# Kernel tuning notes

Measured on AMD Instinct MI355X. Metric: run time of the kernel, lower is better.

Reference implementation:

```python
import jax, jax.numpy as jnp
import numpy as np

WINDOW = 128  # window_size from init_kwargs
D = 1024      # input_dim
S = 8192      # seq_len


def setup_inputs() -> dict:
    key = jax.random.key(0)
    k1, k2, k3, k4, k5 = jax.random.split(key, 5)
    bound = 1.0 / np.sqrt(D)
    x = jax.random.normal(k1, (1, S, D), dtype=jnp.float32)
    Wq = jax.random.uniform(k2, (D, D), minval=-bound, maxval=bound, dtype=jnp.float32)
    bq = jax.random.uniform(k3, (D,), minval=-bound, maxval=bound, dtype=jnp.float32)
    Wk = jax.random.uniform(k4, (D, D), minval=-bound, maxval=bound, dtype=jnp.float32)
    bk = jax.random.uniform(k5, (D,), minval=-bound, maxval=bound, dtype=jnp.float32)
    return {"x": x, "Wq": Wq, "bq": bq, "Wk": Wk, "bk": bk}


def reference(x, Wq, bq, Wk, bk):
    # x: [1, S, D]  (original code only works with batch==1)
    xs = x[0]                          # [S, D]
    q = xs @ Wq.T + bq                 # [S, D]
    k = xs @ Wk.T + bk                 # [S, D]
    scores = q @ k.T                   # [S, S] dense, matches original buffer
    t = jnp.arange(S)[:, None]
    s = jnp.arange(S)[None, :]
    # original writes scores only for s in [t-WINDOW, t+WINDOW); elsewhere stays 0
    inwin = (s >= t - WINDOW) & (s < t + WINDOW)
    scores = jnp.where(inwin, scores, 0.0)
    attn = jax.nn.softmax(scores, axis=1)  # softmax INCLUDES the zero entries, as in original
    out = attn @ xs                    # [S, D]
    return out
```

## Files before the change

### kernel.cpp

```cpp
#include <hip/hip_runtime.h>

#define S 8192
#define D 1024
#define WINDOW 128
#define TQ 16
#define UMAX 288
#define BK 32
#define PAD 68
#define BAND 384

typedef __attribute__((ext_vector_type(8))) short short8;
typedef __attribute__((ext_vector_type(4))) float floatx4;
typedef __attribute__((ext_vector_type(4))) unsigned short ushort4v;
typedef unsigned short u16t;

__device__ __forceinline__ float wave_sum(float v) {
  #pragma unroll
  for (int off = 32; off > 0; off >>= 1) v += __shfl_xor(v, off, 64);
  return v;
}
__device__ __forceinline__ float wave_max(float v) {
  #pragma unroll
  for (int off = 32; off > 0; off >>= 1) v = fmaxf(v, __shfl_xor(v, off, 64));
  return v;
}
__device__ __forceinline__ unsigned int f2bf_rn(float f) {
  unsigned int u = __float_as_uint(f);
  return (u + 0x7fffu + ((u >> 16) & 1u)) >> 16;
}

__global__ __launch_bounds__(256) void uv_kernel(
    const float* __restrict__ Wq, const float* __restrict__ Wk,
    const float* __restrict__ bq, const float* __restrict__ bk,
    float* __restrict__ u, float* __restrict__ v, float* __restrict__ cbuf)
{
  const int i = blockIdx.x * 256 + threadIdx.x;
  const int n0 = blockIdx.y * 128;
  float us = 0.f, vs = 0.f;
  for (int n = n0; n < n0 + 128; ++n) {
    us += Wq[(size_t)n * D + i] * bk[n];
    vs += Wk[(size_t)n * D + i] * bq[n];
  }
  atomicAdd(&u[i], us);
  atomicAdd(&v[i], vs);
  if (blockIdx.x == 0 && blockIdx.y == 0) {
    float cs = 0.f;
    for (int n = threadIdx.x; n < D; n += 256) cs += bq[n] * bk[n];
    atomicAdd(cbuf, cs);
  }
}

__global__ __launch_bounds__(256) void prep_kernel(
    const float* __restrict__ x, const float* __restrict__ u,
    const float* __restrict__ v, u16t* __restrict__ xhi, u16t* __restrict__ xlo,
    u16t* __restrict__ xT, float* __restrict__ xsum,
    float* __restrict__ a, float* __restrict__ b)
{
  __shared__ float tile[64][65];
  const int s0 = blockIdx.x * 64;
  const int d0 = blockIdx.y * 64;
  const int t = threadIdx.x;
  #pragma unroll
  for (int p = 0; p < 4; ++p) {
    int r = (t >> 4) + p * 16;
    int c = (t & 15) * 4;
    float4 vv = *(const float4*)(x + (size_t)(s0 + r) * D + d0 + c);
    float f[4] = {vv.x, vv.y, vv.z, vv.w};
    tile[r][c+0] = vv.x; tile[r][c+1] = vv.y; tile[r][c+2] = vv.z; tile[r][c+3] = vv.w;
    ushort4v h, l;
    #pragma unroll
    for (int e = 0; e < 4; ++e) {
      unsigned int hb = f2bf_rn(f[e]);
      float hf = __uint_as_float(hb << 16);
      h[e] = (u16t)hb;
      l[e] = (u16t)f2bf_rn(f[e] - hf);
    }
    size_t idx = (size_t)(s0 + r) * D + d0 + c;
    *(ushort4v*)(xhi + idx) = h;
    *(ushort4v*)(xlo + idx) = l;
  }
  __syncthreads();
  #pragma unroll
  for (int p = 0; p < 4; ++p) {
    int dd = (t >> 4) + p * 16;
    int ss = (t & 15) * 4;
    ushort4v o;
    #pragma unroll
    for (int e = 0; e < 4; ++e) o[e] = (u16t)f2bf_rn(tile[ss + e][dd]);
    *(ushort4v*)(xT + (size_t)(d0 + dd) * S + s0 + ss) = o;
  }
  if (t < 64) {
    float s = 0.f;
    #pragma unroll 8
    for (int r = 0; r < 64; ++r) s += tile[r][t];
    atomicAdd(&xsum[d0 + t], s);
  } else if (t < 128) {
    int r = t - 64;
    float s = 0.f;
    for (int c = 0; c < 64; ++c) s += tile[r][c] * u[d0 + c];
    atomicAdd(&a[s0 + r], s);
  } else if (t < 192) {
    int r = t - 128;
    float s = 0.f;
    for (int c = 0; c < 64; ++c) s += tile[r][c] * v[d0 + c];
    atomicAdd(&b[s0 + r], s);
  }
}

__global__ __launch_bounds__(256) void transposeW_kernel(
    const float* __restrict__ Wq, const float* __restrict__ Wk,
    u16t* __restrict__ wqth, u16t* __restrict__ wqtl,
    u16t* __restrict__ wkth, u16t* __restrict__ wktl)
{
  __shared__ float tile[64][65];
  const float* W = blockIdx.z ? Wk : Wq;
  u16t* oh = blockIdx.z ? wkth : wqth;
  u16t* ol = blockIdx.z ? wktl : wqtl;
  const int n0 = blockIdx.x * 64;
  const int i0 = blockIdx.y * 64;
  const int t = threadIdx.x;
  #pragma unroll
  for (int p = 0; p < 4; ++p) {
    int r = (t >> 4) + p * 16;
    int c = (t & 15) * 4;
    float4 vv = *(const float4*)(W + (size_t)(n0 + r) * D + i0 + c);
    tile[r][c+0] = vv.x; tile[r][c+1] = vv.y; tile[r][c+2] = vv.z; tile[r][c+3] = vv.w;
  }
  __syncthreads();
  #pragma unroll
  for (int p = 0; p < 4; ++p) {
    int ii = (t >> 4) + p * 16;
    int nn = (t & 15) * 4;
    ushort4v h, l;
    #pragma unroll
    for (int e = 0; e < 4; ++e) {
      float f = tile[nn + e][ii];
      unsigned int hb = f2bf_rn(f);
      float hf = __uint_as_float(hb << 16);
      h[e] = (u16t)hb;
      l[e] = (u16t)f2bf_rn(f - hf);
    }
    size_t idx = (size_t)(i0 + ii) * D + n0 + nn;
    *(ushort4v*)(oh + idx) = h;
    *(ushort4v*)(ol + idx) = l;
  }
}

__global__ __launch_bounds__(256) void m_kernel(
    const u16t* __restrict__ wqth, const u16t* __restrict__ wqtl,
    const u16t* __restrict__ wkth, const u16t* __restrict__ wktl,
    u16t* __restrict__ mh, u16t* __restrict__ ml)
{
  __shared__ __align__(16) u16t Mbuf[4][64 * BK];

  const int tid  = threadIdx.x;
  const int lane = tid & 63;
  const int wv   = tid >> 6;
  const int i0   = blockIdx.x * 64;
  const int j0   = blockIdx.y * 64;

  floatx4 acc[2][2] = {};
  const int m0w = (wv & 1) * 32;
  const int n0w = (wv >> 1) * 32;
  const int srow = lane >> 2;
  const int scol = (lane & 3) * 8;

  for (int k0 = 0; k0 < D; k0 += BK) {
    __syncthreads();
    {
      const u16t* src = (wv == 0) ? wqth : (wv == 1) ? wqtl : (wv == 2) ? wkth : wktl;
      const int base  = (wv < 2) ? i0 : j0;
      #pragma unroll
      for (int sg = 0; sg < 4; ++sg) {
        int row = base + sg * 16 + srow;
        size_t g = (size_t)row * D + k0 + scol;
        __builtin_amdgcn_global_load_lds(
            (const __attribute__((address_space(1))) void*)(src + g),
            (__attribute__((address_space(3))) void*)(&Mbuf[wv][sg * 512]), 16, 0, 0);
      }
    }
    __syncthreads();
    short8 ah[2], al[2], bh[2], bl[2];
    #pragma unroll
    for (int t = 0; t < 2; ++t) {
      int ar = (m0w + t * 16 + (lane & 15)) * BK + (lane >> 4) * 8;
      int br = (n0w + t * 16 + (lane & 15)) * BK + (lane >> 4) * 8;
      ah[t] = *(const short8*)&Mbuf[0][ar];
      al[t] = *(const short8*)&Mbuf[1][ar];
      bh[t] = *(const short8*)&Mbuf[2][br];
      bl[t] = *(const short8*)&Mbuf[3][br];
    }
    #pragma unroll
    for (int mt = 0; mt < 2; ++mt)
      #pragma unroll
      for (int nt = 0; nt < 2; ++nt) {
        acc[mt][nt] = __builtin_amdgcn_mfma_f32_16x16x32_bf16(ah[mt], bh[nt], acc[mt][nt], 0, 0, 0);
        acc[mt][nt] = __builtin_amdgcn_mfma_f32_16x16x32_bf16(ah[mt], bl[nt], acc[mt][nt], 0, 0, 0);
        acc[mt][nt] = __builtin_amdgcn_mfma_f32_16x16x32_bf16(al[mt], bh[nt], acc[mt][nt], 0, 0, 0);
      }
  }
  #pragma unroll
  for (int mt = 0; mt < 2; ++mt)
    #pragma unroll
    for (int nt = 0; nt < 2; ++nt) {
      int j = j0 + n0w + nt * 16 + (lane & 15);
      int i = i0 + m0w + mt * 16 + (lane >> 4) * 4;
      #pragma unroll
      for (int r = 0; r < 4; ++r) {
        float f = acc[mt][nt][r];
        unsigned int hb = f2bf_rn(f);
        float hf = __uint_as_float(hb << 16);
        size_t idx = (size_t)(i + r) * D + j;
        mh[idx] = (u16t)hb;
        ml[idx] = (u16t)f2bf_rn(f - hf);
      }
    }
}

__global__ __launch_bounds__(256) void y_kernel(
    const u16t* __restrict__ xhi, const u16t* __restrict__ xlo,
    const u16t* __restrict__ mhp, const u16t* __restrict__ mlp,
    u16t* __restrict__ yh, u16t* __restrict__ yl)
{
  __shared__ __align__(16) u16t Ah[2 * 128 * BK];
  __shared__ __align__(16) u16t Al[2 * 128 * BK];
  __shared__ __align__(16) u16t Bh[2 * 128 * BK];
  __shared__ __align__(16) u16t Bl[2 * 128 * BK];

  const int tid  = threadIdx.x;
  const int lane = tid & 63;
  const int wv   = tid >> 6;
  const int s0   = blockIdx.x * 128;
  const int i0   = blockIdx.y * 128;

  floatx4 acc[4][4] = {};
  const int m0w  = (wv & 1) * 64;
  const int n0w  = (wv >> 1) * 64;
  const int srow = lane >> 2;
  const int scol = (lane & 3) * 8;

  for (int k0 = 0; k0 < D; k0 += 64) {
    __syncthreads();
    #pragma unroll
    for (int h = 0; h < 2; ++h) {
      #pragma unroll
      for (int sg = 0; sg < 2; ++sg) {
        int seg  = wv * 2 + sg;
        int arow = s0 + seg * 16 + srow;
        int brow = i0 + seg * 16 + srow;
        size_t ga = (size_t)arow * D + k0 + h * 32 + scol;
        size_t gb = (size_t)brow * D + k0 + h * 32 + scol;
        int lb = h * 4096 + seg * 512;
        __builtin_amdgcn_global_load_lds(
            (const __attribute__((address_space(1))) void*)(xhi + ga),
            (__attribute__((address_space(3))) void*)(&Ah[lb]), 16, 0, 0);
        __builtin_amdgcn_global_load_lds(
            (const __attribute__((address_space(1))) void*)(xlo + ga),
            (__attribute__((address_space(3))) void*)(&Al[lb]), 16, 0, 0);
        __builtin_amdgcn_global_load_lds(
            (const __attribute__((address_space(1))) void*)(mhp + gb),
            (__attribute__((address_space(3))) void*)(&Bh[lb]), 16, 0, 0);
        __builtin_amdgcn_global_load_lds(
            (const __attribute__((address_space(1))) void*)(mlp + gb),
            (__attribute__((address_space(3))) void*)(&Bl[lb]), 16, 0, 0);
      }
    }
    __syncthreads();
    #pragma unroll
    for (int h = 0; h < 2; ++h) {
      short8 ah[4], al[4], bh[4], bl[4];
      #pragma unroll
      for (int t = 0; t < 4; ++t) {
        int ar = h * 4096 + (m0w + t * 16 + (lane & 15)) * BK + (lane >> 4) * 8;
        int br = h * 4096 + (n0w + t * 16 + (lane & 15)) * BK + (lane >> 4) * 8;
        ah[t] = *(const short8*)&Ah[ar];
        al[t] = *(const short8*)&Al[ar];
        bh[t] = *(const short8*)&Bh[br];
        bl[t] = *(const short8*)&Bl[br];
      }
      #pragma unroll
      for (int mt = 0; mt < 4; ++mt)
        #pragma unroll
        for (int nt = 0; nt < 4; ++nt) {
          acc[mt][nt] = __builtin_amdgcn_mfma_f32_16x16x32_bf16(ah[mt], bh[nt], acc[mt][nt], 0, 0, 0);
          acc[mt][nt] = __builtin_amdgcn_mfma_f32_16x16x32_bf16(ah[mt], bl[nt], acc[mt][nt], 0, 0, 0);
          acc[mt][nt] = __builtin_amdgcn_mfma_f32_16x16x32_bf16(al[mt], bh[nt], acc[mt][nt], 0, 0, 0);
        }
    }
  }
  #pragma unroll
  for (int mt = 0; mt < 4; ++mt)
    #pragma unroll
    for (int nt = 0; nt < 4; ++nt) {
      int i = i0 + n0w + nt * 16 + (lane & 15);
      int s = s0 + m0w + mt * 16 + (lane >> 4) * 4;
      #pragma unroll
      for (int r = 0; r < 4; ++r) {
        float f = acc[mt][nt][r];
        unsigned int hb = f2bf_rn(f);
        float hf = __uint_as_float(hb << 16);
        size_t idx = (size_t)(s + r) * D + i;
        yh[idx] = (u16t)hb;
        yl[idx] = (u16t)f2bf_rn(f - hf);
      }
    }
}

__global__ __launch_bounds__(256) void scores_kernel(
    const u16t* __restrict__ xhi, const u16t* __restrict__ xlo,
    const u16t* __restrict__ yh, const u16t* __restrict__ yl,
    const float* __restrict__ a, const float* __restrict__ b,
    const float* __restrict__ cbuf, float* __restrict__ band)
{
  __shared__ __align__(16) u16t Ah[2 * 128 * BK];
  __shared__ __align__(16) u16t Al[2 * 128 * BK];
  __shared__ __align__(16) u16t Bh[2 * 128 * BK];
  __shared__ __align__(16) u16t Bl[2 * 128 * BK];

  const int tid  = threadIdx.x;
  const int lane = tid & 63;
  const int wv   = tid >> 6;
  const int t0   = blockIdx.x * 128;
  const int jt   = blockIdx.y;
  const int s_base = t0 - 128 + jt * 128;
  const float cval = cbuf[0];

  floatx4 acc[4][4] = {};
  const int m0w  = (wv & 1) * 64;
  const int n0w  = (wv >> 1) * 64;
  const int srow = lane >> 2;
  const int scol = (lane & 3) * 8;

  for (int k0 = 0; k0 < D; k0 += 64) {
    __syncthreads();
    #pragma unroll
    for (int h = 0; h < 2; ++h) {
      #pragma unroll
      for (int sg = 0; sg < 2; ++sg) {
        int seg  = wv * 2 + sg;
        int arow = t0 + seg * 16 + srow;
        int brow = s_base + seg * 16 + srow;
        brow = min(max(brow, 0), S - 1);
        size_t ga = (size_t)arow * D + k0 + h * 32 + scol;
        size_t gb = (size_t)brow * D + k0 + h * 32 + scol;
        int lb = h * 4096 + seg * 512;
        __builtin_amdgcn_global_load_lds(
            (const __attribute__((address_space(1))) void*)(xhi + ga),
            (__attribute__((address_space(3))) void*)(&Ah[lb]), 16, 0, 0);
        __builtin_amdgcn_global_load_lds(
            (const __attribute__((address_space(1))) void*)(xlo + ga),
            (__attribute__((address_space(3))) void*)(&Al[lb]), 16, 0, 0);
        __builtin_amdgcn_global_load_lds(
            (const __attribute__((address_space(1))) void*)(yh + gb),
            (__attribute__((address_space(3))) void*)(&Bh[lb]), 16, 0, 0);
        __builtin_amdgcn_global_load_lds(
            (const __attribute__((address_space(1))) void*)(yl + gb),
            (__attribute__((address_space(3))) void*)(&Bl[lb]), 16, 0, 0);
      }
    }
    __syncthreads();
    #pragma unroll
    for (int h = 0; h < 2; ++h) {
      short8 ah[4], al[4], bh[4], bl[4];
      #pragma unroll
      for (int t = 0; t < 4; ++t) {
        int ar = h * 4096 + (m0w + t * 16 + (lane & 15)) * BK + (lane >> 4) * 8;
        int br = h * 4096 + (n0w + t * 16 + (lane & 15)) * BK + (lane >> 4) * 8;
        ah[t] = *(const short8*)&Ah[ar];
        al[t] = *(const short8*)&Al[ar];
        bh[t] = *(const short8*)&Bh[br];
        bl[t] = *(const short8*)&Bl[br];
      }
      #pragma unroll
      for (int mt = 0; mt < 4; ++mt)
        #pragma unroll
        for (int nt = 0; nt < 4; ++nt) {
          acc[mt][nt] = __builtin_amdgcn_mfma_f32_16x16x32_bf16(ah[mt], bh[nt], acc[mt][nt], 0, 0, 0);
          acc[mt][nt] = __builtin_amdgcn_mfma_f32_16x16x32_bf16(ah[mt], bl[nt], acc[mt][nt], 0, 0, 0);
          acc[mt][nt] = __builtin_amdgcn_mfma_f32_16x16x32_bf16(al[mt], bh[nt], acc[mt][nt], 0, 0, 0);
        }
    }
  }
  #pragma unroll
  for (int mt = 0; mt < 4; ++mt)
    #pragma unroll
    for (int nt = 0; nt < 4; ++nt) {
      int n_loc = n0w + nt * 16 + (lane & 15);
      int s = s_base + n_loc;
      float bv = (s >= 0 && s < S) ? b[s] : 0.f;
      #pragma unroll
      for (int r = 0; r < 4; ++r) {
        int m_loc = m0w + mt * 16 + (lane >> 4) * 4 + r;
        int t = t0 + m_loc;
        bool inwin = (s >= t - WINDOW) && (s < t + WINDOW) && (s >= 0) && (s < S);
        float sv = inwin ? (acc[mt][nt][r] + a[t] + bv + cval) : 0.f;
        band[(size_t)t * BAND + jt * 128 + n_loc] = sv;
      }
    }
}

__global__ __launch_bounds__(256) void softmax_kernel(
    const float* __restrict__ band, u16t* __restrict__ Pb, float* __restrict__ e0d)
{
  const int lane = threadIdx.x & 63;
  const int w    = threadIdx.x >> 6;
  const int t    = blockIdx.x * 4 + w;
  const float* row = band + (size_t)t * BAND;
  float v[6];
  float mx = 0.f;
  #pragma unroll
  for (int i = 0; i < 6; ++i) {
    v[i] = row[i * 64 + lane];
    mx = fmaxf(mx, v[i]);
  }
  mx = wave_max(mx);
  float e0 = __expf(-mx);
  float ss = 0.f;
  #pragma unroll
  for (int i = 0; i < 6; ++i) {
    v[i] = __expf(v[i] - mx);
    ss += v[i];
  }
  ss = wave_sum(ss);
  float dinv = 1.f / (ss + (float)(S - BAND) * e0);
  #pragma unroll
  for (int i = 0; i < 6; ++i)
    Pb[(size_t)t * BAND + i * 64 + lane] = (u16t)f2bf_rn((v[i] - e0) * dinv);
  if (lane == 0) e0d[t] = e0 * dinv;
}

__global__ __launch_bounds__(256) void pv_kernel(
    const u16t* __restrict__ Pb, const u16t* __restrict__ xT,
    const float* __restrict__ e0d, const float* __restrict__ xsum,
    float* __restrict__ out)
{
  __shared__ __align__(16) u16t Ab[2 * 128 * BK];
  __shared__ __align__(16) u16t Bb[2 * 128 * BK];

  const int tid  = threadIdx.x;
  const int lane = tid & 63;
  const int wv   = tid >> 6;
  const int t0   = blockIdx.x * 128;
  const int d0   = blockIdx.y * 128;
  const int origin = t0 - 128;

  floatx4 acc[4][4] = {};
  const int m0w  = (wv & 1) * 64;
  const int n0w  = (wv >> 1) * 64;
  const int srow = lane >> 2;
  const int scol = (lane & 3) * 8;

  for (int k0 = 0; k0 < BAND; k0 += 64) {
    __syncthreads();
    #pragma unroll
    for (int h = 0; h < 2; ++h) {
      #pragma unroll
      for (int sg = 0; sg < 2; ++sg) {
        int seg  = wv * 2 + sg;
        int arow = t0 + seg * 16 + srow;
        int brow = d0 + seg * 16 + srow;
        int s_g  = origin + k0 + h * 32 + scol;
        s_g = min(max(s_g, 0), S - 8);
        size_t ga = (size_t)arow * BAND + k0 + h * 32 + scol;
        size_t gb = (size_t)brow * S + s_g;
        int lb = h * 4096 + seg * 512;
        __builtin_amdgcn_global_load_lds(
            (const __attribute__((address_space(1))) void*)(Pb + ga),
            (__attribute__((address_space(3))) void*)(&Ab[lb]), 16, 0, 0);
        __builtin_amdgcn_global_load_lds(
            (const __attribute__((address_space(1))) void*)(xT + gb),
            (__attribute__((address_space(3))) void*)(&Bb[lb]), 16, 0, 0);
      }
    }
    __syncthreads();
    #pragma unroll
    for (int h = 0; h < 2; ++h) {
      short8 af[4], bf[4];
      #pragma unroll
      for (int t = 0; t < 4; ++t) {
        int ar = h * 4096 + (m0w + t * 16 + (lane & 15)) * BK + (lane >> 4) * 8;
        int br = h * 4096 + (n0w + t * 16 + (lane & 15)) * BK + (lane >> 4) * 8;
        af[t] = *(const short8*)&Ab[ar];
        bf[t] = *(const short8*)&Bb[br];
      }
      #pragma unroll
      for (int mt = 0; mt < 4; ++mt)
        #pragma unroll
        for (int nt = 0; nt < 4; ++nt)
          acc[mt][nt] = __builtin_amdgcn_mfma_f32_16x16x32_bf16(af[mt], bf[nt], acc[mt][nt], 0, 0, 0);
    }
  }
  #pragma unroll
  for (int mt = 0; mt < 4; ++mt)
    #pragma unroll
    for (int nt = 0; nt < 4; ++nt) {
      int n_g = d0 + n0w + nt * 16 + (lane & 15);
      float xs = xsum[n_g];
      #pragma unroll
      for (int r = 0; r < 4; ++r) {
        int m_g = t0 + m0w + mt * 16 + (lane >> 4) * 4 + r;
        out[(size_t)m_g * D + n_g] = acc[mt][nt][r] + e0d[m_g] * xs;
      }
    }
}

__global__ __launch_bounds__(256) void proj_kernel(
    const float* __restrict__ x, const float* __restrict__ Wq,
    const float* __restrict__ bqv, const float* __restrict__ Wk,
    const float* __restrict__ bkv, float* __restrict__ qout,
    float* __restrict__ kout)
{
  __shared__ __align__(16) float xs[BK][PAD];
  __shared__ __align__(16) float wqs[BK][PAD];
  __shared__ __align__(16) float wks[BK][PAD];
  const int tid = threadIdx.x;
  const int tx = tid & 15, ty = tid >> 4;
  const int t0 = blockIdx.x * 64, i0 = blockIdx.y * 64;
  float accq[4][4] = {}, acck[4][4] = {};
  const int lrow0 = tid >> 3, lc4 = (tid & 7) * 4;
  for (int k0 = 0; k0 < D; k0 += BK) {
    __syncthreads();
    #pragma unroll
    for (int p = 0; p < 2; ++p) {
      int row = lrow0 + p * 32;
      float4 a = *(const float4*)(x  + (size_t)(t0 + row) * D + k0 + lc4);
      float4 b = *(const float4*)(Wq + (size_t)(i0 + row) * D + k0 + lc4);
      float4 c = *(const float4*)(Wk + (size_t)(i0 + row) * D + k0 + lc4);
      xs [lc4+0][row]=a.x; xs [lc4+1][row]=a.y; xs [lc4+2][row]=a.z; xs [lc4+3][row]=a.w;
      wqs[lc4+0][row]=b.x; wqs[lc4+1][row]=b.y; wqs[lc4+2][row]=b.z; wqs[lc4+3][row]=b.w;
      wks[lc4+0][row]=c.x; wks[lc4+1][row]=c.y; wks[lc4+2][row]=c.z; wks[lc4+3][row]=c.w;
    }
    __syncthreads();
    #pragma unroll
    for (int kk = 0; kk < BK; ++kk) {
      float4 av = *(const float4*)&xs [kk][ty*4];
      float4 bv = *(const float4*)&wqs[kk][tx*4];
      float4 cv = *(const float4*)&wks[kk][tx*4];
      float a[4] = {av.x, av.y, av.z, av.w};
      float b[4] = {bv.x, bv.y, bv.z, bv.w};
      float c[4] = {cv.x, cv.y, cv.z, cv.w};
      #pragma unroll
      for (int r = 0; r < 4; ++r)
        #pragma unroll
        for (int cc = 0; cc < 4; ++cc) {
          accq[r][cc] = fmaf(a[r], b[cc], accq[r][cc]);
          acck[r][cc] = fmaf(a[r], c[cc], acck[r][cc]);
        }
    }
  }
  float4 bq4 = *(const float4*)(bqv + i0 + tx*4);
  float4 bk4 = *(const float4*)(bkv + i0 + tx*4);
  #pragma unroll
  for (int r = 0; r < 4; ++r) {
    int trow = t0 + ty*4 + r;
    float4 oq = { accq[r][0]+bq4.x, accq[r][1]+bq4.y, accq[r][2]+bq4.z, accq[r][3]+bq4.w };
    float4 ok = { acck[r][0]+bk4.x, acck[r][1]+bk4.y, acck[r][2]+bk4.z, acck[r][3]+bk4.w };
    *(float4*)(qout + (size_t)trow * D + i0 + tx*4) = oq;
    *(float4*)(kout + (size_t)trow * D + i0 + tx*4) = ok;
  }
}

__global__ __launch_bounds__(256) void colsum_kernel(const float* __restrict__ x,
                                                     float* __restrict__ xsum)
{
  int d = blockIdx.x * 256 + threadIdx.x;
  int tbase = blockIdx.y * 256;
  float s = 0.f;
  for (int t = 0; t < 256; ++t) s += x[(size_t)(tbase + t) * D + d];
  atomicAdd(&xsum[d], s);
}

__global__ __launch_bounds__(256) void attn_kernel(
    const float* __restrict__ x, const float* __restrict__ q,
    const float* __restrict__ kmat, const float* __restrict__ xsum,
    float* __restrict__ out)
{
  __shared__ __align__(16) float scl[TQ][UMAX];
  __shared__ float e0s[TQ], dinv[TQ];
  const int tid = threadIdx.x, lane = tid & 63, wv = tid >> 6;
  const int t0 = blockIdx.x * TQ;
  const int lo_u = max(0, t0 - WINDOW);
  const int hi_u = min(S, t0 + TQ - 1 + WINDOW);
  const int ucnt = hi_u - lo_u;
  for (int i = tid; i < TQ * UMAX; i += 256) (&scl[0][0])[i] = 0.f;
  __syncthreads();
  {
    const int tiB = wv * 4;
    float4 qf[4][4];
    #pragma unroll
    for (int g = 0; g < 4; ++g) {
      int t = t0 + tiB + g;
      #pragma unroll
      for (int j = 0; j < 4; ++j)
        qf[g][j] = *(const float4*)(q + (size_t)t * D + lane*4 + j*256);
    }
    const int wlo = max(0, t0 + tiB - WINDOW);
    const int whi = min(S, t0 + tiB + 3 + WINDOW);
    for (int s = wlo; s < whi; ++s) {
      float4 kf[4];
      #pragma unroll
      for (int j = 0; j < 4; ++j)
        kf[j] = *(const float4*)(kmat + (size_t)s * D + lane*4 + j*256);
      float acc[4];
      #pragma unroll
      for (int g = 0; g < 4; ++g) {
        float v = 0.f;
        #pragma unroll
        for (int j = 0; j < 4; ++j) {
          v = fmaf(qf[g][j].x, kf[j].x, v);
          v = fmaf(qf[g][j].y, kf[j].y, v);
          v = fmaf(qf[g][j].z, kf[j].z, v);
          v = fmaf(qf[g][j].w, kf[j].w, v);
        }
        acc[g] = v;
      }
      #pragma unroll
      for (int g = 0; g < 4; ++g) {
        float tot = wave_sum(acc[g]);
        int t = t0 + tiB + g;
        if (lane == 0 && s >= t - WINDOW && s < t + WINDOW)
          scl[tiB + g][s - lo_u] = tot;
      }
    }
  }
  __syncthreads();
  #pragma unroll
  for (int g = 0; g < 4; ++g) {
    int ti = wv * 4 + g;
    int t = t0 + ti;
    int lo = max(0, t - WINDOW), hi = min(S, t + WINDOW);
    int cnt = hi - lo, off = lo - lo_u;
    float m = 0.f;
    for (int i = lane; i < cnt; i += 64) m = fmaxf(m, scl[ti][off + i]);
    m = wave_max(m);
    float e0 = __expf(-m);
    float ssum = 0.f;
    for (int i = lane; i < cnt; i += 64) {
      float e = __expf(scl[ti][off + i] - m);
      ssum += e;
      scl[ti][off + i] = e - e0;
    }
    ssum = wave_sum(ssum);
    if (lane == 0) {
      dinv[ti] = 1.f / (ssum + (float)(S - cnt) * e0);
      e0s[ti] = e0;
    }
  }
  __syncthreads();
  {
    const int c4 = tid * 4;
    float4 acc[TQ];
    #pragma unroll
    for (int ti = 0; ti < TQ; ++ti) acc[ti] = make_float4(0.f, 0.f, 0.f, 0.f);
    for (int su = 0; su < ucnt; su += 4) {
      float4 xr[4];
      #pragma unroll
      for (int u = 0; u < 4; ++u)
        xr[u] = *(const float4*)(x + (size_t)(lo_u + su + u) * D + c4);
      #pragma unroll
      for (int ti = 0; ti < TQ; ++ti) {
        float4 w4 = *(const float4*)&scl[ti][su];
        float wvv[4] = {w4.x, w4.y, w4.z, w4.w};
        #pragma unroll
        for (int u = 0; u < 4; ++u) {
          acc[ti].x = fmaf(wvv[u], xr[u].x, acc[ti].x);
          acc[ti].y = fmaf(wvv[u], xr[u].y, acc[ti].y);
          acc[ti].z = fmaf(wvv[u], xr[u].z, acc[ti].z);
          acc[ti].w = fmaf(wvv[u], xr[u].w, acc[ti].w);
        }
      }
    }
    float4 xsv = *(const float4*)(xsum + c4);
    #pragma unroll
    for (int ti = 0; ti < TQ; ++ti) {
      float e0 = e0s[ti], di = dinv[ti];
      float4 o;
      o.x = (acc[ti].x + e0 * xsv.x) * di;
      o.y = (acc[ti].y + e0 * xsv.y) * di;
      o.z = (acc[ti].z + e0 * xsv.z) * di;
      o.w = (acc[ti].w + e0 * xsv.w) * di;
      *(float4*)(out + (size_t)(t0 + ti) * D + c4) = o;
    }
  }
}

extern "C" void kernel_launch(void* const* d_in, const int* in_sizes, int n_in,
                              void* d_out, int out_size, void* d_ws, size_t ws_size,
                              hipStream_t stream) {
  const float* x  = (const float*)d_in[0];
  const float* Wq = (const float*)d_in[1];
  const float* bq = (const float*)d_in[2];
  const float* Wk = (const float*)d_in[3];
  const float* bk = (const float*)d_in[4];
  float* outp = (float*)d_out;

  const size_t SD = (size_t)S * D;
  const size_t DD = (size_t)D * D;

  float* xsum = (float*)d_ws;
  float* u    = xsum + D;
  float* v    = u + D;
  float* a    = v + D;
  float* b    = a + S;
  float* cbuf = b + S;
  size_t zero_bytes = (size_t)(3 * D + 2 * S + 16) * sizeof(float);

  u16t* xhi  = (u16t*)(cbuf + 16);
  u16t* xlo  = xhi + SD;
  u16t* xT   = xlo + SD;
  u16t* wqth = xT + SD;
  u16t* wqtl = wqth + DD;
  u16t* wkth = wqtl + DD;
  u16t* wktl = wkth + DD;
  u16t* mh   = wktl + DD;
  u16t* ml   = mh + DD;
  u16t* yh   = ml + DD;
  u16t* yl   = yh + SD;
  float* band = (float*)(yl + SD);
  u16t*  Pb   = (u16t*)(band + (size_t)S * BAND);
  float* e0d  = (float*)(Pb + (size_t)S * BAND);
  size_t needed = (size_t)((char*)(e0d + S) - (char*)d_ws);

  if (ws_size >= needed) {
    (void)hipMemsetAsync(d_ws, 0, zero_bytes, stream);
    uv_kernel<<<dim3(D / 256, 8), 256, 0, stream>>>(Wq, Wk, bq, bk, u, v, cbuf);
    prep_kernel<<<dim3(S / 64, D / 64), 256, 0, stream>>>(x, u, v, xhi, xlo, xT, xsum, a, b);
    transposeW_kernel<<<dim3(D / 64, D / 64, 2), 256, 0, stream>>>(Wq, Wk, wqth, wqtl, wkth, wktl);
    m_kernel<<<dim3(D / 64, D / 64), 256, 0, stream>>>(wqth, wqtl, wkth, wktl, mh, ml);
    y_kernel<<<dim3(S / 128, D / 128), 256, 0, stream>>>(xhi, xlo, mh, ml, yh, yl);
    scores_kernel<<<dim3(S / 128, 3), 256, 0, stream>>>(xhi, xlo, yh, yl, a, b, cbuf, band);
    softmax_kernel<<<S / 4, 256, 0, stream>>>(band, Pb, e0d);
    pv_kernel<<<dim3(S / 128, D / 128), 256, 0, stream>>>(Pb, xT, e0d, xsum, outp);
  } else {
    float* xs2  = (float*)d_ws;
    float* q    = xs2 + D;
    float* kbuf = q + SD;
    (void)hipMemsetAsync(xs2, 0, D * sizeof(float), stream);
    colsum_kernel<<<dim3(D / 256, S / 256), 256, 0, stream>>>(x, xs2);
    proj_kernel<<<dim3(S / 64, D / 64), 256, 0, stream>>>(x, Wq, bq, Wk, bk, q, kbuf);
    attn_kernel<<<S / TQ, 256, 0, stream>>>(x, q, kbuf, xs2, outp);
  }
}
```

Measured before the change: 259.3 us.

## Shrink band to 320 with 64-row tiles and swizzle LDS layouts

Cuts the query tile in the scores and PV kernels from 128 to 64 rows, so the stored score band per row shrinks from 384 to 320 columns (5 tiles of 64). This removes band columns that never fall in the window, saving QK, softmax and PV work, and doubles the grid for more parallelism. It also adds an XOR swizzle to the LDS staging and read offsets in the m, y, scores and PV GEMMs to reduce bank conflicts. The smaller tiles give less operand reuse per block.

```diff
diff --git a/kernel.cpp b/kernel.cpp
--- a/kernel.cpp
+++ b/kernel.cpp
@@ -7,7 +7,7 @@
 #define UMAX 288
 #define BK 32
 #define PAD 68
-#define BAND 384
+#define BAND 320
 
 typedef __attribute__((ext_vector_type(8))) short short8;
 typedef __attribute__((ext_vector_type(4))) float floatx4;
@@ -28,6 +28,7 @@
   unsigned int u = __float_as_uint(f);
   return (u + 0x7fffu + ((u >> 16) & 1u)) >> 16;
 }
+
 
 __global__ __launch_bounds__(256) void uv_kernel(
     const float* __restrict__ Wq, const float* __restrict__ Wk,
@@ -163,7 +164,8 @@
   const int m0w = (wv & 1) * 32;
   const int n0w = (wv >> 1) * 32;
   const int srow = lane >> 2;
-  const int scol = (lane & 3) * 8;
+  const int scolw = ((lane & 3) ^ ((lane >> 3) & 3)) * 8;
+  const int rs    = (((lane >> 4) ^ ((lane >> 1) & 3)) * 8);
 
   for (int k0 = 0; k0 < D; k0 += BK) {
     __syncthreads();
@@ -173,7 +175,7 @@
       #pragma unroll
       for (int sg = 0; sg < 4; ++sg) {
         int row = base + sg * 16 + srow;
-        size_t g = (size_t)row * D + k0 + scol;
+        size_t g = (size_t)row * D + k0 + scolw;
         __builtin_amdgcn_global_load_lds(
             (const __attribute__((address_space(1))) void*)(src + g),
             (__attribute__((address_space(3))) void*)(&Mbuf[wv][sg * 512]), 16, 0, 0);
@@ -183,8 +185,8 @@
     short8 ah[2], al[2], bh[2], bl[2];
     #pragma unroll
     for (int t = 0; t < 2; ++t) {
-      int ar = (m0w + t * 16 + (lane & 15)) * BK + (lane >> 4) * 8;
-      int br = (n0w + t * 16 + (lane & 15)) * BK + (lane >> 4) * 8;
+      int ar = (m0w + t * 16 + (lane & 15)) * BK + rs;
+      int br = (n0w + t * 16 + (lane & 15)) * BK + rs;
       ah[t] = *(const short8*)&Mbuf[0][ar];
       al[t] = *(const short8*)&Mbuf[1][ar];
       bh[t] = *(const short8*)&Mbuf[2][br];
@@ -237,7 +239,8 @@
   const int m0w  = (wv & 1) * 64;
   const int n0w  = (wv >> 1) * 64;
   const int srow = lane >> 2;
-  const int scol = (lane & 3) * 8;
+  const int scolw = ((lane & 3) ^ ((lane >> 3) & 3)) * 8;
+  const int rs    = (((lane >> 4) ^ ((lane >> 1) & 3)) * 8);
 
   for (int k0 = 0; k0 < D; k0 += 64) {
     __syncthreads();
@@ -248,8 +251,8 @@
         int seg  = wv * 2 + sg;
         int arow = s0 + seg * 16 + srow;
         int brow = i0 + seg * 16 + srow;
-        size_t ga = (size_t)arow * D + k0 + h * 32 + scol;
-        size_t gb = (size_t)brow * D + k0 + h * 32 + scol;
+        size_t ga = (size_t)arow * D + k0 + h * 32 + scolw;
+        size_t gb = (size_t)brow * D + k0 + h * 32 + scolw;
         int lb = h * 4096 + seg * 512;
         __builtin_amdgcn_global_load_lds(
             (const __attribute__((address_space(1))) void*)(xhi + ga),
@@ -271,8 +274,8 @@
       short8 ah[4], al[4], bh[4], bl[4];
       #pragma unroll
       for (int t = 0; t < 4; ++t) {
-        int ar = h * 4096 + (m0w + t * 16 + (lane & 15)) * BK + (lane >> 4) * 8;
-        int br = h * 4096 + (n0w + t * 16 + (lane & 15)) * BK + (lane >> 4) * 8;
+        int ar = h * 4096 + (m0w + t * 16 + (lane & 15)) * BK + rs;
+        int br = h * 4096 + (n0w + t * 16 + (lane & 15)) * BK + rs;
         ah[t] = *(const short8*)&Ah[ar];
         al[t] = *(const short8*)&Al[ar];
         bh[t] = *(const short8*)&Bh[br];
@@ -312,69 +315,66 @@
     const float* __restrict__ a, const float* __restrict__ b,
     const float* __restrict__ cbuf, float* __restrict__ band)
 {
-  __shared__ __align__(16) u16t Ah[2 * 128 * BK];
-  __shared__ __align__(16) u16t Al[2 * 128 * BK];
-  __shared__ __align__(16) u16t Bh[2 * 128 * BK];
-  __shared__ __align__(16) u16t Bl[2 * 128 * BK];
+  __shared__ __align__(16) u16t Ah[2 * 64 * BK];
+  __shared__ __align__(16) u16t Al[2 * 64 * BK];
+  __shared__ __align__(16) u16t Bh[2 * 64 * BK];
+  __shared__ __align__(16) u16t Bl[2 * 64 * BK];
 
   const int tid  = threadIdx.x;
   const int lane = tid & 63;
   const int wv   = tid >> 6;
-  const int t0   = blockIdx.x * 128;
+  const int t0   = blockIdx.x * 64;
   const int jt   = blockIdx.y;
-  const int s_base = t0 - 128 + jt * 128;
+  const int s_base = t0 - 128 + jt * 64;
   const float cval = cbuf[0];
 
-  floatx4 acc[4][4] = {};
-  const int m0w  = (wv & 1) * 64;
-  const int n0w  = (wv >> 1) * 64;
+  floatx4 acc[2][2] = {};
+  const int m0w  = (wv & 1) * 32;
+  const int n0w  = (wv >> 1) * 32;
   const int srow = lane >> 2;
-  const int scol = (lane & 3) * 8;
+  const int scolw = ((lane & 3) ^ ((lane >> 3) & 3)) * 8;
+  const int rs    = (((lane >> 4) ^ ((lane >> 1) & 3)) * 8);
 
   for (int k0 = 0; k0 < D; k0 += 64) {
     __syncthreads();
     #pragma unroll
     for (int h = 0; h < 2; ++h) {
-      #pragma unroll
-      for (int sg = 0; sg < 2; ++sg) {
-        int seg  = wv * 2 + sg;
-        int arow = t0 + seg * 16 + srow;
-        int brow = s_base + seg * 16 + srow;
-        brow = min(max(brow, 0), S - 1);
-        size_t ga = (size_t)arow * D + k0 + h * 32 + scol;
-        size_t gb = (size_t)brow * D + k0 + h * 32 + scol;
-        int lb = h * 4096 + seg * 512;
-        __builtin_amdgcn_global_load_lds(
-            (const __attribute__((address_space(1))) void*)(xhi + ga),
-            (__attribute__((address_space(3))) void*)(&Ah[lb]), 16, 0, 0);
-        __builtin_amdgcn_global_load_lds(
-            (const __attribute__((address_space(1))) void*)(xlo + ga),
-            (__attribute__((address_space(3))) void*)(&Al[lb]), 16, 0, 0);
-        __builtin_amdgcn_global_load_lds(
-            (const __attribute__((address_space(1))) void*)(yh + gb),
-            (__attribute__((address_space(3))) void*)(&Bh[lb]), 16, 0, 0);
-        __builtin_amdgcn_global_load_lds(
-            (const __attribute__((address_space(1))) void*)(yl + gb),
-            (__attribute__((address_space(3))) void*)(&Bl[lb]), 16, 0, 0);
-      }
+      int arow = t0 + wv * 16 + srow;
+      int brow = s_base + wv * 16 + srow;
+      brow = min(max(brow, 0), S - 1);
+      size_t ga = (size_t)arow * D + k0 + h * 32 + scolw;
+      size_t gb = (size_t)brow * D + k0 + h * 32 + scolw;
+      int lb = h * 2048 + wv * 512;
+      __builtin_amdgcn_global_load_lds(
+          (const __attribute__((address_space(1))) void*)(xhi + ga),
+          (__attribute__((address_space(3))) void*)(&Ah[lb]), 16, 0, 0);
+      __builtin_amdgcn_global_load_lds(
+          (const __attribute__((address_space(1))) void*)(xlo + ga),
+          (__attribute__((address_space(3))) void*)(&Al[lb]), 16, 0, 0);
+      __builtin_amdgcn_global_load_lds(
+          (const __attribute__((address_space(1))) void*)(yh + gb),
+          (__attribute__((address_space(3))) void*)(&Bh[lb]), 16, 0, 0);
+      __builtin_amdgcn_global_load_lds(
+          (const __attribute__((address_space(1))) void*)(yl + gb),
+          (__attribute__((address_space(3))) void*)(&Bl[lb]), 16, 0, 0);
     }
     __syncthreads();
     #pragma unroll
     for (int h = 0; h < 2; ++h) {
-      short8 ah[4], al[4], bh[4], bl[4];
-      #pragma unroll
-      for (int t = 0; t < 4; ++t) {
-        int ar = h * 4096 + (m0w + t * 16 + (lane & 15)) * BK + (lane >> 4) * 8;
-        int br = h * 4096 + (n0w + t * 16 + (lane & 15)) * BK + (lane >> 4) * 8;
+      short8 ah[2], al[2], bh[2], bl[2];
+      #pragma unroll
+      for (int t = 0; t < 2; ++t) {
+        int ar = h * 2048 + (m0w + t * 16 + (lane & 15)) * BK + rs;
+        int br = h * 2048 + (n0w + t * 16 + (lane & 15)) * BK + rs;
         ah[t] = *(const short8*)&Ah[ar];
         al[t] = *(const short8*)&Al[ar];
         bh[t] = *(const short8*)&Bh[br];
         bl[t] = *(const short8*)&Bl[br];
       }
       #pragma unroll
-      for (int mt = 0; mt < 4; ++mt)
+      for (int mt = 0; mt < 2; ++mt)
         #pragma unroll
-        for (int nt = 0; nt < 4; ++nt) {
+        for (int nt = 0; nt < 2; ++nt) {
           acc[mt][nt] = __builtin_amdgcn_mfma_f32_16x16x32_bf16(ah[mt], bh[nt], acc[mt][nt], 0, 0, 0);
           acc[mt][nt] = __builtin_amdgcn_mfma_f32_16x16x32_bf16(ah[mt], bl[nt], acc[mt][nt], 0, 0, 0);
           acc[mt][nt] = __builtin_amdgcn_mfma_f32_16x16x32_bf16(al[mt], bh[nt], acc[mt][nt], 0, 0, 0);
@@ -382,9 +382,9 @@
     }
   }
   #pragma unroll
-  for (int mt = 0; mt < 4; ++mt)
-    #pragma unroll
-    for (int nt = 0; nt < 4; ++nt) {
+  for (int mt = 0; mt < 2; ++mt)
+    #pragma unroll
+    for (int nt = 0; nt < 2; ++nt) {
       int n_loc = n0w + nt * 16 + (lane & 15);
       int s = s_base + n_loc;
       float bv = (s >= 0 && s < S) ? b[s] : 0.f;
@@ -394,7 +394,7 @@
         int t = t0 + m_loc;
         bool inwin = (s >= t - WINDOW) && (s < t + WINDOW) && (s >= 0) && (s < S);
         float sv = inwin ? (acc[mt][nt][r] + a[t] + bv + cval) : 0.f;
-        band[(size_t)t * BAND + jt * 128 + n_loc] = sv;
+        band[(size_t)t * BAND + jt * 64 + n_loc] = sv;
       }
     }
 }
@@ -406,10 +406,10 @@
   const int w    = threadIdx.x >> 6;
   const int t    = blockIdx.x * 4 + w;
   const float* row = band + (size_t)t * BAND;
-  float v[6];
+  float v[5];
   float mx = 0.f;
   #pragma unroll
-  for (int i = 0; i < 6; ++i) {
+  for (int i = 0; i < 5; ++i) {
     v[i] = row[i * 64 + lane];
     mx = fmaxf(mx, v[i]);
   }
@@ -417,14 +417,14 @@
   float e0 = __expf(-mx);
   float ss = 0.f;
   #pragma unroll
-  for (int i = 0; i < 6; ++i) {
+  for (int i = 0; i < 5; ++i) {
     v[i] = __expf(v[i] - mx);
     ss += v[i];
   }
   ss = wave_sum(ss);
   float dinv = 1.f / (ss + (float)(S - BAND) * e0);
   #pragma unroll
-  for (int i = 0; i < 6; ++i)
+  for (int i = 0; i < 5; ++i)
     Pb[(size_t)t * BAND + i * 64 + lane] = (u16t)f2bf_rn((v[i] - e0) * dinv);
   if (lane == 0) e0d[t] = e0 * dinv;
 }
@@ -434,40 +434,44 @@
     const float* __restrict__ e0d, const float* __restrict__ xsum,
     float* __restrict__ out)
 {
-  __shared__ __align__(16) u16t Ab[2 * 128 * BK];
+  __shared__ __align__(16) u16t Ab[2 * 64 * BK];
   __shared__ __align__(16) u16t Bb[2 * 128 * BK];
 
   const int tid  = threadIdx.x;
   const int lane = tid & 63;
   const int wv   = tid >> 6;
-  const int t0   = blockIdx.x * 128;
+  const int t0   = blockIdx.x * 64;
   const int d0   = blockIdx.y * 128;
   const int origin = t0 - 128;
 
-  floatx4 acc[4][4] = {};
-  const int m0w  = (wv & 1) * 64;
+  floatx4 acc[2][4] = {};
+  const int m0w  = (wv & 1) * 32;
   const int n0w  = (wv >> 1) * 64;
   const int srow = lane >> 2;
-  const int scol = (lane & 3) * 8;
+  const int scolw = ((lane & 3) ^ ((lane >> 3) & 3)) * 8;
+  const int rs    = (((lane >> 4) ^ ((lane >> 1) & 3)) * 8);
 
   for (int k0 = 0; k0 < BAND; k0 += 64) {
     __syncthreads();
     #pragma unroll
     for (int h = 0; h < 2; ++h) {
+      {
+        int arow = t0 + wv * 16 + srow;
+        size_t ga = (size_t)arow * BAND + k0 + h * 32 + scolw;
+        int lb = h * 2048 + wv * 512;
+        __builtin_amdgcn_global_load_lds(
+            (const __attribute__((address_space(1))) void*)(Pb + ga),
+            (__attribute__((address_space(3))) void*)(&Ab[lb]), 16, 0, 0);
+      }
       #pragma unroll
       for (int sg = 0; sg < 2; ++sg) {
         int seg  = wv * 2 + sg;
-        int arow = t0 + seg * 16 + srow;
         int brow = d0 + seg * 16 + srow;
-        int s_g  = origin + k0 + h * 32 + scol;
+        int s_g  = origin + k0 + h * 32 + scolw;
         s_g = min(max(s_g, 0), S - 8);
-        size_t ga = (size_t)arow * BAND + k0 + h * 32 + scol;
         size_t gb = (size_t)brow * S + s_g;
         int lb = h * 4096 + seg * 512;
         __builtin_amdgcn_global_load_lds(
-            (const __attribute__((address_space(1))) void*)(Pb + ga),
-            (__attribute__((address_space(3))) void*)(&Ab[lb]), 16, 0, 0);
-        __builtin_amdgcn_global_load_lds(
             (const __attribute__((address_space(1))) void*)(xT + gb),
             (__attribute__((address_space(3))) void*)(&Bb[lb]), 16, 0, 0);
       }
@@ -475,23 +479,26 @@
     __syncthreads();
     #pragma unroll
     for (int h = 0; h < 2; ++h) {
-      short8 af[4], bf[4];
+      short8 af[2], bf[4];
+      #pragma unroll
+      for (int t = 0; t < 2; ++t) {
+        int ar = h * 2048 + (m0w + t * 16 + (lane & 15)) * BK + rs;
+        af[t] = *(const short8*)&Ab[ar];
+      }
       #pragma unroll
       for (int t = 0; t < 4; ++t) {
-        int ar = h * 4096 + (m0w + t * 16 + (lane & 15)) * BK + (lane >> 4) * 8;
-        int br = h * 4096 + (n0w + t * 16 + (lane & 15)) * BK + (lane >> 4) * 8;
-        af[t] = *(const short8*)&Ab[ar];
+        int br = h * 4096 + (n0w + t * 16 + (lane & 15)) * BK + rs;
         bf[t] = *(const short8*)&Bb[br];
       }
       #pragma unroll
-      for (int mt = 0; mt < 4; ++mt)
+      for (int mt = 0; mt < 2; ++mt)
         #pragma unroll
         for (int nt = 0; nt < 4; ++nt)
           acc[mt][nt] = __builtin_amdgcn_mfma_f32_16x16x32_bf16(af[mt], bf[nt], acc[mt][nt], 0, 0, 0);
     }
   }
   #pragma unroll
-  for (int mt = 0; mt < 4; ++mt)
+  for (int mt = 0; mt < 2; ++mt)
     #pragma unroll
     for (int nt = 0; nt < 4; ++nt) {
       int n_g = d0 + n0w + nt * 16 + (lane & 15);
@@ -728,9 +735,9 @@
     transposeW_kernel<<<dim3(D / 64, D / 64, 2), 256, 0, stream>>>(Wq, Wk, wqth, wqtl, wkth, wktl);
     m_kernel<<<dim3(D / 64, D / 64), 256, 0, stream>>>(wqth, wqtl, wkth, wktl, mh, ml);
     y_kernel<<<dim3(S / 128, D / 128), 256, 0, stream>>>(xhi, xlo, mh, ml, yh, yl);
-    scores_kernel<<<dim3(S / 128, 3), 256, 0, stream>>>(xhi, xlo, yh, yl, a, b, cbuf, band);
+    scores_kernel<<<dim3(S / 64, 5), 256, 0, stream>>>(xhi, xlo, yh, yl, a, b, cbuf, band);
     softmax_kernel<<<S / 4, 256, 0, stream>>>(band, Pb, e0d);
-    pv_kernel<<<dim3(S / 128, D / 128), 256, 0, stream>>>(Pb, xT, e0d, xsum, outp);
+    pv_kernel<<<dim3(S / 64, D / 128), 256, 0, stream>>>(Pb, xT, e0d, xsum, outp);
   } else {
     float* xs2  = (float*)d_ws;
     float* q    = xs2 + D;
```

After: 264.6 us. +2.0%, slower.
